# Optimization experiments

Measured on AMD Instinct MI355X. Metric: run time of the kernel, lower is better.

Reference implementation:

```python
import jax, jax.numpy as jnp
import numpy as np

N_NODES = 50000
N_EDGES = 1_600_000
F_IN = 128
HID = 64
HEADS = 4
NCLS = 2
NEG_SLOPE = 0.2  # PyG GATConv default


def setup_inputs() -> dict:
    key = jax.random.key(0)
    ks = jax.random.split(key, 12)
    s = 0.1
    return {
        "x": jax.random.normal(ks[0], (N_NODES, F_IN), jnp.float32),
        "edge_index": jax.random.randint(ks[1], (2, N_EDGES), 0, N_NODES, jnp.int32),
        "W1": jax.random.normal(ks[2], (F_IN, HEADS * HID), jnp.float32) * s,
        "att_src1": jax.random.normal(ks[3], (HEADS, HID), jnp.float32) * s,
        "att_dst1": jax.random.normal(ks[4], (HEADS, HID), jnp.float32) * s,
        "b1": jnp.zeros((HEADS * HID,), jnp.float32),
        "W2": jax.random.normal(ks[5], (HEADS * HID, HID), jnp.float32) * s,
        "att_src2": jax.random.normal(ks[6], (1, HID), jnp.float32) * s,
        "att_dst2": jax.random.normal(ks[7], (1, HID), jnp.float32) * s,
        "b2": jnp.zeros((HID,), jnp.float32),
        "Wc": jax.random.normal(ks[8], (HID, NCLS), jnp.float32) * s,
        "bc": jnp.zeros((NCLS,), jnp.float32),
    }


def _gat_layer(x, src, dst, W, a_src, a_dst, bias, heads, out_ch, concat):
    """Faithful PyG GATConv (eval mode): gather, LeakyReLU score, segment softmax by dst, scatter-add."""
    n = x.shape[0]
    h = (x @ W).reshape(n, heads, out_ch)            # [N, H, C]
    alpha_s = (h * a_src).sum(-1)                    # [N, H]
    alpha_d = (h * a_dst).sum(-1)                    # [N, H]
    e = jax.nn.leaky_relu(alpha_s[src] + alpha_d[dst], NEG_SLOPE)  # [E, H]
    e_max = jax.ops.segment_max(e, dst, num_segments=n)
    ex = jnp.exp(e - e_max[dst])
    denom = jax.ops.segment_sum(ex, dst, num_segments=n)
    coef = ex / (denom[dst] + 1e-16)                 # [E, H]
    out = jax.ops.segment_sum(h[src] * coef[:, :, None], dst, num_segments=n)  # [N, H, C]
    out = out.reshape(n, heads * out_ch) if concat else out.mean(axis=1)
    return out + bias


def reference(x, edge_index, W1, att_src1, att_dst1, b1, W2, att_src2, att_dst2, b2, Wc, bc):
    n = x.shape[0]
    loop = jnp.arange(n, dtype=edge_index.dtype)     # GATConv add_self_loops=True
    src = jnp.concatenate([edge_index[0], loop])
    dst = jnp.concatenate([edge_index[1], loop])
    h1 = jax.nn.elu(_gat_layer(x, src, dst, W1, att_src1, att_dst1, b1, HEADS, HID, True))
    # dropout p=0.6 is identity in eval mode
    h2 = jax.nn.elu(_gat_layer(h1, src, dst, W2, att_src2, att_dst2, b2, 1, HID, False))
    pooled = h2.mean(axis=0, keepdims=True)          # batch=None path: [1, HID]
    return pooled @ Wc + bc                          # [1, NCLS]
```

## Files before the change

### kernel.cpp

```cpp
#include <hip/hip_runtime.h>
#include <cstdint>
#include <cstddef>

#define NEG_SLOPE 0.2f
#define F_IN 128
#define C1 256
#define HID 64
#define HEADS 4
#define LOG2E 1.4426950408889634f
#define NBUCK 196
#define BCAP 10240

typedef __attribute__((ext_vector_type(8))) short bf16x8;
typedef __attribute__((ext_vector_type(4))) float f32x4;
typedef __attribute__((ext_vector_type(2))) float f32x2;

__device__ __forceinline__ float wave_reduce_sum(float v) {
#pragma unroll
  for (int off = 32; off > 0; off >>= 1) v += __shfl_down(v, off);
  return v;
}

__device__ __forceinline__ unsigned short f2bf(float f) {
  union { float f; unsigned int u; } v; v.f = f;
  unsigned int u = v.u;
  unsigned int r = (u + 0x7fffu + ((u >> 16) & 1u)) >> 16;
  return (unsigned short)r;
}
__device__ __forceinline__ float bf_lo(unsigned int u) { return __uint_as_float(u << 16); }
__device__ __forceinline__ float bf_hi(unsigned int u) { return __uint_as_float(u & 0xffff0000u); }

__device__ __forceinline__ unsigned char f2fp8(float f) {
  int p = __builtin_amdgcn_cvt_pk_fp8_f32(f, f, 0, false);
  return (unsigned char)(p & 0xff);
}

__global__ __launch_bounds__(256) void setup_kernel(const float* __restrict__ W1,
                                                    const float* __restrict__ W2,
                                                    unsigned short* __restrict__ W1b,
                                                    unsigned short* __restrict__ W2b,
                                                    int* __restrict__ gcursor,
                                                    float* __restrict__ poolrep) {
  const int TOT = 256 + 4096 + 32768 + 16384;
  for (int idx = threadIdx.x + blockIdx.x * 256; idx < TOT; idx += 256 * gridDim.x) {
    if (idx < 256) {
      gcursor[idx] = 0;
    } else if (idx < 256 + 4096) {
      poolrep[idx - 256] = 0.f;
    } else if (idx < 256 + 4096 + 32768) {
      int o = idx - (256 + 4096);
      int head = o >> 13, ks = (o >> 11) & 3, nt = (o >> 9) & 3;
      int lane = (o >> 3) & 63, j = o & 7;
      int k = ks * 32 + (lane >> 4) * 8 + j;
      int c = head * 64 + nt * 16 + (lane & 15);
      W1b[o] = f2bf(W1[k * 256 + c]);
    } else {
      int o = idx - (256 + 4096 + 32768);
      int ks = o >> 11, nt = (o >> 9) & 3, lane = (o >> 3) & 63, j = o & 7;
      int k = ks * 32 + (lane >> 4) * 8 + j;
      int c = nt * 16 + (lane & 15);
      W2b[o] = f2bf(W2[k * 64 + c]);
    }
  }
}

__global__ __launch_bounds__(256) void gemm1_mfma(const float* __restrict__ Af,
                                                  const unsigned short* __restrict__ Wb,
                                                  unsigned char* __restrict__ H8,
                                                  float* __restrict__ as_out,
                                                  float* __restrict__ ad_out,
                                                  const float* __restrict__ att_s,
                                                  const float* __restrict__ att_d,
                                                  int M) {
  constexpr int KSTEPS = 4, NH = HEADS, K = 128, N = 256;
  const int lane = threadIdx.x & 63, wid = threadIdx.x >> 6;
  const int rowbase = blockIdx.x * 64 + wid * 16;
  const int g = lane >> 4, li = lane & 15;
  int r_a = rowbase + li;
  if (r_a > M - 1) r_a = M - 1;

  f32x4 acc[NH][4];
#pragma unroll
  for (int h = 0; h < NH; h++)
#pragma unroll
    for (int nt = 0; nt < 4; nt++) {
      acc[h][nt][0] = 0.f; acc[h][nt][1] = 0.f; acc[h][nt][2] = 0.f; acc[h][nt][3] = 0.f;
    }

#pragma unroll
  for (int ks = 0; ks < KSTEPS; ks++) {
    bf16x8 a;
    const float* p = Af + (size_t)r_a * K + ks * 32 + g * 8;
    float4 v0 = *(const float4*)p, v1 = *(const float4*)(p + 4);
    a[0] = (short)f2bf(v0.x); a[1] = (short)f2bf(v0.y);
    a[2] = (short)f2bf(v0.z); a[3] = (short)f2bf(v0.w);
    a[4] = (short)f2bf(v1.x); a[5] = (short)f2bf(v1.y);
    a[6] = (short)f2bf(v1.z); a[7] = (short)f2bf(v1.w);
#pragma unroll
    for (int h = 0; h < NH; h++)
#pragma unroll
      for (int nt = 0; nt < 4; nt++) {
        bf16x8 b = *(const bf16x8*)(Wb + ((size_t)((h * KSTEPS + ks) * 4 + nt) * 64 + lane) * 8);
        acc[h][nt] = __builtin_amdgcn_mfma_f32_16x16x32_bf16(a, b, acc[h][nt], 0, 0, 0);
      }
  }

#pragma unroll
  for (int h = 0; h < NH; h++) {
    float asum[4] = {0.f, 0.f, 0.f, 0.f}, dsum[4] = {0.f, 0.f, 0.f, 0.f};
#pragma unroll
    for (int nt = 0; nt < 4; nt++) {
      float ws = att_s[h * 64 + nt * 16 + li];
      float wd = att_d[h * 64 + nt * 16 + li];
#pragma unroll
      for (int r = 0; r < 4; r++) { asum[r] += acc[h][nt][r] * ws; dsum[r] += acc[h][nt][r] * wd; }
    }
#pragma unroll
    for (int r = 0; r < 4; r++) {
#pragma unroll
      for (int m = 1; m < 16; m <<= 1) {
        asum[r] += __shfl_xor(asum[r], m);
        dsum[r] += __shfl_xor(dsum[r], m);
      }
    }
#pragma unroll
    for (int r = 0; r < 4; r++) {
      int gr = rowbase + g * 4 + r;
      if (gr < M) {
#pragma unroll
        for (int nt = 0; nt < 4; nt++)
          H8[(size_t)gr * N + h * 64 + nt * 16 + li] = f2fp8(acc[h][nt][r]);
        if (li == 0) {
          as_out[(size_t)gr * NH + h] = asum[r] * LOG2E;
          ad_out[(size_t)gr * NH + h] = dsum[r] * LOG2E;
        }
      }
    }
  }
}

__global__ __launch_bounds__(256) void partition_kernel(const int* __restrict__ esrc,
                                                        const int* __restrict__ edst,
                                                        int* __restrict__ gcursor,
                                                        int2* __restrict__ pairs,
                                                        int E, int Etot) {
  __shared__ int hist[256];
  __shared__ int base[256];
  const int tid = threadIdx.x;
  const int e0 = blockIdx.x * 2048;
  hist[tid] = 0;
  __syncthreads();
  int d8[8], rk8[8], bk8[8];
#pragma unroll
  for (int j = 0; j < 8; j++) {
    int e = e0 + tid * 8 + j;
    d8[j] = -1;
    if (e < Etot) {
      int d = (e < E) ? edst[e] : (e - E);
      d8[j] = d;
      bk8[j] = d >> 8;
      rk8[j] = atomicAdd(&hist[bk8[j]], 1);
    }
  }
  __syncthreads();
  if (hist[tid] > 0) base[tid] = atomicAdd(&gcursor[tid], hist[tid]);
  __syncthreads();
#pragma unroll
  for (int j = 0; j < 8; j++) {
    int e = e0 + tid * 8 + j;
    if (e < Etot) {
      int s = (e < E) ? esrc[e] : (e - E);
      int2 pr; pr.x = s; pr.y = d8[j];
      pairs[(size_t)bk8[j] * BCAP + base[bk8[j]] + rk8[j]] = pr;
    }
  }
}

__global__ __launch_bounds__(512) void bucket_csr(const int2* __restrict__ pairs,
                                                  const int* __restrict__ gcursor,
                                                  const float4* __restrict__ as1,
                                                  const float4* __restrict__ ad1,
                                                  int4* __restrict__ recs,
                                                  int* __restrict__ row_ptr,
                                                  int N, int Etot) {
  __shared__ int hist[256], offs[256], cnt2[256], gpre[256];
  const int b = blockIdx.x;
  const int tid = threadIdx.x;
  if (tid < 256) {
    hist[tid] = 0; cnt2[tid] = 0;
    gpre[tid] = (tid < NBUCK) ? gcursor[tid] : 0;
  }
  __syncthreads();
  for (int off = 1; off < 256; off <<= 1) {
    int t = 0;
    if (tid < 256 && tid >= off) t = gpre[tid - off];
    __syncthreads();
    if (tid < 256) gpre[tid] += t;
    __syncthreads();
  }
  const int cnt = gcursor[b];
  const int gbase = (b == 0) ? 0 : gpre[b - 1];
  const int2* bp = pairs + (size_t)b * BCAP;
  if (b == 0 && tid == 0) row_ptr[N] = Etot;

  for (int i = tid; i < cnt; i += 512) atomicAdd(&hist[bp[i].y & 255], 1);
  __syncthreads();
  if (tid < 256) offs[tid] = hist[tid];
  __syncthreads();
  for (int off = 1; off < 256; off <<= 1) {
    int t = 0;
    if (tid < 256 && tid >= off) t = offs[tid - off];
    __syncthreads();
    if (tid < 256) offs[tid] += t;
    __syncthreads();
  }
  if (tid < 256) {
    int node = b * 256 + tid;
    if (node < N) row_ptr[node] = gbase + offs[tid] - hist[tid];
  }
  __syncthreads();
  for (int i = tid; i < cnt; i += 512) {
    int2 pr = bp[i];
    int lo = pr.y & 255;
    int rank = atomicAdd(&cnt2[lo], 1);
    int pos = gbase + offs[lo] - hist[lo] + rank;
    float4 a = as1[pr.x], dd = ad1[pr.y];
    float s0 = a.x + dd.x, s1 = a.y + dd.y, s2 = a.z + dd.z, s3 = a.w + dd.w;
    float w0 = exp2f(fmaxf(s0, NEG_SLOPE * s0));
    float w1 = exp2f(fmaxf(s1, NEG_SLOPE * s1));
    float w2 = exp2f(fmaxf(s2, NEG_SLOPE * s2));
    float w3 = exp2f(fmaxf(s3, NEG_SLOPE * s3));
    int4 r;
    r.x = pr.x;
    r.y = (int)((unsigned)f2bf(w0) | ((unsigned)f2bf(w1) << 16));
    r.z = (int)((unsigned)f2bf(w2) | ((unsigned)f2bf(w3) << 16));
    r.w = 0;
    recs[pos] = r;
  }
}

__global__ __launch_bounds__(256) void agg1_gemm2(const unsigned char* __restrict__ H8,
                                                  const int4* __restrict__ recs,
                                                  const int* __restrict__ row_ptr,
                                                  const float* __restrict__ b1,
                                                  const unsigned short* __restrict__ W2b,
                                                  const float* __restrict__ att_s2,
                                                  const float* __restrict__ att_d2,
                                                  unsigned char* __restrict__ H2,
                                                  float* __restrict__ as2,
                                                  float* __restrict__ ad2, int n) {
  __shared__ unsigned char lds_h[16 * 512];
  __shared__ float pA[4][16], pD[4][16];
  const int tid = threadIdx.x;
  const int l = tid & 63, w = tid >> 6;
  const int dbase = blockIdx.x * 16;
  const int hh = l >> 4;
  const int shamt = (hh & 1) ? 0 : 16;
  const bool lowpair = hh < 2;
  const float4 bb = *(const float4*)(b1 + l * 4);

#define WSEL(r) __uint_as_float(((unsigned)((lowpair) ? (r).y : (r).z) << shamt) & 0xffff0000u)
#define ACCUM(wgt, u8)                                                     \
  {                                                                        \
    f32x2 lo_ = __builtin_amdgcn_cvt_pk_f32_fp8((int)(u8), false);         \
    f32x2 hi_ = __builtin_amdgcn_cvt_pk_f32_fp8((int)(u8), true);          \
    accA += lo_ * (wgt); accB += hi_ * (wgt);                              \
    denom += (wgt);                                                        \
  }
  for (int i = 0; i < 4; i++) {
    int dloc = w * 4 + i;
    int d = dbase + dloc;
    bool active = d < n;
    f32x2 accA = {0.f, 0.f}, accB = {0.f, 0.f};
    float denom = 0.f;
    if (active) {
      int e0 = __builtin_amdgcn_readfirstlane(row_ptr[d]);
      int e1 = __builtin_amdgcn_readfirstlane(row_ptr[d + 1]);
      int e = e0;
      for (; e + 3 < e1; e += 4) {
        int4 r0 = recs[e], r1 = recs[e + 1], r2 = recs[e + 2], r3 = recs[e + 3];
        unsigned u0 = *(const unsigned*)(H8 + (size_t)r0.x * C1 + l * 4);
        unsigned u1 = *(const unsigned*)(H8 + (size_t)r1.x * C1 + l * 4);
        unsigned u2 = *(const unsigned*)(H8 + (size_t)r2.x * C1 + l * 4);
        unsigned u3 = *(const unsigned*)(H8 + (size_t)r3.x * C1 + l * 4);
        float w0 = WSEL(r0), w1 = WSEL(r1), w2 = WSEL(r2), w3 = WSEL(r3);
        ACCUM(w0, u0) ACCUM(w1, u1) ACCUM(w2, u2) ACCUM(w3, u3)
      }
      for (; e < e1; e++) {
        int4 r0 = recs[e];
        unsigned u = *(const unsigned*)(H8 + (size_t)r0.x * C1 + l * 4);
        float wq = WSEL(r0);
        ACCUM(wq, u)
      }
    }
    float inv = 1.f / (denom + 1e-16f);
    float4 o;
    o.x = accA[0] * inv + bb.x; o.y = accA[1] * inv + bb.y;
    o.z = accB[0] * inv + bb.z; o.w = accB[1] * inv + bb.w;
    o.x = o.x > 0.f ? o.x : (__expf(o.x) - 1.f);
    o.y = o.y > 0.f ? o.y : (__expf(o.y) - 1.f);
    o.z = o.z > 0.f ? o.z : (__expf(o.z) - 1.f);
    o.w = o.w > 0.f ? o.w : (__expf(o.w) - 1.f);
    if (!active) { o.x = 0.f; o.y = 0.f; o.z = 0.f; o.w = 0.f; }
    uint2 pk;
    pk.x = (unsigned int)f2bf(o.x) | ((unsigned int)f2bf(o.y) << 16);
    pk.y = (unsigned int)f2bf(o.z) | ((unsigned int)f2bf(o.w) << 16);
    unsigned byte = (unsigned)(l * 8) ^ ((unsigned)(dloc & 7) << 4);
    *(uint2*)(lds_h + dloc * 512 + byte) = pk;
  }
#undef ACCUM
#undef WSEL
  __syncthreads();

  const int li2 = l & 15, g2 = l >> 4;
  f32x4 acc2;
  acc2[0] = 0.f; acc2[1] = 0.f; acc2[2] = 0.f; acc2[3] = 0.f;
#pragma unroll
  for (int ks = 0; ks < 8; ks++) {
    unsigned byte = (unsigned)((ks * 32 + g2 * 8) * 2) ^ ((unsigned)(li2 & 7) << 4);
    bf16x8 a = *(const bf16x8*)(lds_h + li2 * 512 + byte);
    bf16x8 b = *(const bf16x8*)(W2b + ((size_t)(ks * 4 + w) * 64 + l) * 8);
    acc2 = __builtin_amdgcn_mfma_f32_16x16x32_bf16(a, b, acc2, 0, 0, 0);
  }

  float ws = att_s2[w * 16 + li2], wd = att_d2[w * 16 + li2];
  float asum[4], dsum[4];
#pragma unroll
  for (int r = 0; r < 4; r++) { asum[r] = acc2[r] * ws; dsum[r] = acc2[r] * wd; }
#pragma unroll
  for (int r = 0; r < 4; r++) {
#pragma unroll
    for (int m = 1; m < 16; m <<= 1) {
      asum[r] += __shfl_xor(asum[r], m);
      dsum[r] += __shfl_xor(dsum[r], m);
    }
  }
#pragma unroll
  for (int r = 0; r < 4; r++) {
    int row = g2 * 4 + r;
    int d2 = dbase + row;
    if (d2 < n) H2[(size_t)d2 * HID + w * 16 + li2] = f2fp8(acc2[r]);
    if (li2 == 0) { pA[w][row] = asum[r]; pD[w][row] = dsum[r]; }
  }
  __syncthreads();
  if (tid < 16) {
    int d2 = dbase + tid;
    if (d2 < n) as2[d2] = (pA[0][tid] + pA[1][tid] + pA[2][tid] + pA[3][tid]) * LOG2E;
  } else if (tid < 32) {
    int row = tid - 16;
    int d2 = dbase + row;
    if (d2 < n) ad2[d2] = (pD[0][row] + pD[1][row] + pD[2][row] + pD[3][row]) * LOG2E;
  }
}

__global__ __launch_bounds__(256) void agg2_pool(const unsigned char* __restrict__ H2,
                                                 const float* __restrict__ as_,
                                                 const float* __restrict__ ad_,
                                                 const int* __restrict__ row_ptr,
                                                 const int4* __restrict__ recs,
                                                 const float* __restrict__ b2,
                                                 float* __restrict__ poolrep, int n) {
  __shared__ float lds[4][64];
  int wid = threadIdx.x >> 6;
  int d = blockIdx.x * 4 + wid;
  int l = threadIdx.x & 63, q = l >> 4, li = l & 15;
  float ad = ad_[d];
  int e0 = row_ptr[d], e1 = row_ptr[d + 1];
  f32x2 accA = {0.f, 0.f}, accB = {0.f, 0.f};
  float denom = 0.f;
  for (int e = e0 + q; e < e1; e += 4) {
    int s = ((const int*)recs)[(size_t)e * 4];
    float sc = as_[s] + ad;
    float w = exp2f(fmaxf(sc, NEG_SLOPE * sc));
    denom += w;
    unsigned u = *(const unsigned*)(H2 + (size_t)s * HID + li * 4);
    f32x2 lo_ = __builtin_amdgcn_cvt_pk_f32_fp8((int)u, false);
    f32x2 hi_ = __builtin_amdgcn_cvt_pk_f32_fp8((int)u, true);
    accA += lo_ * w; accB += hi_ * w;
  }
#pragma unroll
  for (int m = 16; m <= 32; m <<= 1) {
    accA[0] += __shfl_xor(accA[0], m); accA[1] += __shfl_xor(accA[1], m);
    accB[0] += __shfl_xor(accB[0], m); accB[1] += __shfl_xor(accB[1], m);
    denom += __shfl_xor(denom, m);
  }
  if (q == 0) {
    float inv = 1.f / (denom + 1e-16f);
    float o[4] = {accA[0] * inv + b2[li * 4], accA[1] * inv + b2[li * 4 + 1],
                  accB[0] * inv + b2[li * 4 + 2], accB[1] * inv + b2[li * 4 + 3]};
#pragma unroll
    for (int j = 0; j < 4; j++) {
      float v = o[j];
      lds[wid][li * 4 + j] = v > 0.f ? v : (__expf(v) - 1.f);
    }
  }
  __syncthreads();
  if (threadIdx.x < 64) {
    int c = threadIdx.x;
    float v = lds[0][c] + lds[1][c] + lds[2][c] + lds[3][c];
    atomicAdd(&poolrep[(blockIdx.x & 63) * 64 + c], v);
  }
}

__global__ __launch_bounds__(64) void head_kernel(const float* __restrict__ poolrep,
                                                  const float* __restrict__ Wc,
                                                  const float* __restrict__ bc,
                                                  float* __restrict__ out, float inv_n) {
  int l = threadIdx.x;
  float p = 0.f;
  for (int k = 0; k < 64; k++) p += poolrep[k * 64 + l];
  p *= inv_n;
  float o0 = wave_reduce_sum(p * Wc[l * 2 + 0]);
  float o1 = wave_reduce_sum(p * Wc[l * 2 + 1]);
  if (l == 0) { out[0] = o0 + bc[0]; out[1] = o1 + bc[1]; }
}

static inline size_t align256(size_t x) { return (x + 255) & ~(size_t)255; }

extern "C" void kernel_launch(void* const* d_in, const int* in_sizes, int n_in,
                              void* d_out, int out_size, void* d_ws, size_t ws_size,
                              hipStream_t stream) {
  const float* x        = (const float*)d_in[0];
  const int*   ei       = (const int*)d_in[1];
  const float* W1       = (const float*)d_in[2];
  const float* att_src1 = (const float*)d_in[3];
  const float* att_dst1 = (const float*)d_in[4];
  const float* b1       = (const float*)d_in[5];
  const float* W2       = (const float*)d_in[6];
  const float* att_src2 = (const float*)d_in[7];
  const float* att_dst2 = (const float*)d_in[8];
  const float* b2       = (const float*)d_in[9];
  const float* Wc       = (const float*)d_in[10];
  const float* bc       = (const float*)d_in[11];
  float* out = (float*)d_out;

  const int N = in_sizes[0] / F_IN;
  const int E = in_sizes[1] / 2;
  const int Etot = E + N;
  const int* ei_src = ei;
  const int* ei_dst = ei + E;

  char* w = (char*)d_ws;
  size_t off = 0;
  unsigned char* h1b8 = (unsigned char*)(w + off); off += align256((size_t)N * C1);
  unsigned char* h2b8 = (unsigned char*)(w + off); off += align256((size_t)N * HID);
  float* as1   = (float*)(w + off); off += align256((size_t)N * HEADS * 4);
  float* ad1   = (float*)(w + off); off += align256((size_t)N * HEADS * 4);
  float* as2   = (float*)(w + off); off += align256((size_t)N * 4);
  float* ad2   = (float*)(w + off); off += align256((size_t)N * 4);
  int* row_ptr = (int*)(w + off);   off += align256((size_t)(N + 1) * 4);
  int* gcursor = (int*)(w + off);   off += align256(256 * 4);
  float* poolrep = (float*)(w + off); off += align256(64 * 64 * 4);
  unsigned short* W1b = (unsigned short*)(w + off); off += align256(32768 * 2);
  unsigned short* W2b = (unsigned short*)(w + off); off += align256(16384 * 2);
  int2* pairs  = (int2*)(w + off);  off += align256((size_t)NBUCK * BCAP * 8);
  int4* recs   = (int4*)(w + off);  off += align256((size_t)Etot * 16);

  int nb4 = (N + 3) / 4;
  int rowblocks = (N + 63) / 64;
  int pblocks = (Etot + 2047) / 2048;
  int fblocks = (N + 15) / 16;

  setup_kernel<<<104, 256, 0, stream>>>(W1, W2, W1b, W2b, gcursor, poolrep);
  partition_kernel<<<pblocks, 256, 0, stream>>>(ei_src, ei_dst, gcursor, pairs, E, Etot);
  gemm1_mfma<<<rowblocks, 256, 0, stream>>>(x, W1b, h1b8, as1, ad1,
                                            att_src1, att_dst1, N);
  bucket_csr<<<NBUCK, 512, 0, stream>>>(pairs, gcursor,
                                        (const float4*)as1, (const float4*)ad1,
                                        recs, row_ptr, N, Etot);
  agg1_gemm2<<<fblocks, 256, 0, stream>>>(h1b8, recs, row_ptr, b1, W2b,
                                          att_src2, att_dst2, h2b8, as2, ad2, N);
  agg2_pool<<<nb4, 256, 0, stream>>>(h2b8, as2, ad2, row_ptr, recs, b2, poolrep, N);
  head_kernel<<<1, 64, 0, stream>>>(poolrep, Wc, bc, out, 1.0f / (float)N);
}
```

Baseline: 213.7 us.

## Compress edge records into 16-bit source and packed weight arrays

```diff
diff --git a/kernel.cpp b/kernel.cpp
--- a/kernel.cpp
+++ b/kernel.cpp
@@ -14,6 +14,7 @@
 typedef __attribute__((ext_vector_type(8))) short bf16x8;
 typedef __attribute__((ext_vector_type(4))) float f32x4;
 typedef __attribute__((ext_vector_type(2))) float f32x2;
+typedef unsigned long long ull;
 
 __device__ __forceinline__ float wave_reduce_sum(float v) {
 #pragma unroll
@@ -27,8 +28,6 @@
   unsigned int r = (u + 0x7fffu + ((u >> 16) & 1u)) >> 16;
   return (unsigned short)r;
 }
-__device__ __forceinline__ float bf_lo(unsigned int u) { return __uint_as_float(u << 16); }
-__device__ __forceinline__ float bf_hi(unsigned int u) { return __uint_as_float(u & 0xffff0000u); }
 
 __device__ __forceinline__ unsigned char f2fp8(float f) {
   int p = __builtin_amdgcn_cvt_pk_fp8_f32(f, f, 0, false);
@@ -142,7 +141,7 @@
 __global__ __launch_bounds__(256) void partition_kernel(const int* __restrict__ esrc,
                                                         const int* __restrict__ edst,
                                                         int* __restrict__ gcursor,
-                                                        int2* __restrict__ pairs,
+                                                        unsigned* __restrict__ pairs,
                                                         int E, int Etot) {
   __shared__ int hist[256];
   __shared__ int base[256];
@@ -170,17 +169,18 @@
     int e = e0 + tid * 8 + j;
     if (e < Etot) {
       int s = (e < E) ? esrc[e] : (e - E);
-      int2 pr; pr.x = s; pr.y = d8[j];
-      pairs[(size_t)bk8[j] * BCAP + base[bk8[j]] + rk8[j]] = pr;
-    }
-  }
-}
-
-__global__ __launch_bounds__(512) void bucket_csr(const int2* __restrict__ pairs,
+      unsigned pk = (unsigned)s | ((unsigned)(d8[j] & 255) << 16);
+      __builtin_nontemporal_store(pk, &pairs[(size_t)bk8[j] * BCAP + base[bk8[j]] + rk8[j]]);
+    }
+  }
+}
+
+__global__ __launch_bounds__(512) void bucket_csr(const unsigned* __restrict__ pairs,
                                                   const int* __restrict__ gcursor,
                                                   const float4* __restrict__ as1,
                                                   const float4* __restrict__ ad1,
-                                                  int4* __restrict__ recs,
+                                                  unsigned short* __restrict__ src16,
+                                                  ull* __restrict__ w4,
                                                   int* __restrict__ row_ptr,
                                                   int N, int Etot) {
   __shared__ int hist[256], offs[256], cnt2[256], gpre[256];
@@ -200,10 +200,13 @@
   }
   const int cnt = gcursor[b];
   const int gbase = (b == 0) ? 0 : gpre[b - 1];
-  const int2* bp = pairs + (size_t)b * BCAP;
+  const unsigned* bp = pairs + (size_t)b * BCAP;
   if (b == 0 && tid == 0) row_ptr[N] = Etot;
 
-  for (int i = tid; i < cnt; i += 512) atomicAdd(&hist[bp[i].y & 255], 1);
+  for (int i = tid; i < cnt; i += 512) {
+    unsigned p = __builtin_nontemporal_load(&bp[i]);
+    atomicAdd(&hist[p >> 16], 1);
+  }
   __syncthreads();
   if (tid < 256) offs[tid] = hist[tid];
   __syncthreads();
@@ -220,27 +223,27 @@
   }
   __syncthreads();
   for (int i = tid; i < cnt; i += 512) {
-    int2 pr = bp[i];
-    int lo = pr.y & 255;
+    unsigned p = __builtin_nontemporal_load(&bp[i]);
+    int lo = (int)(p >> 16);
+    int src = (int)(p & 0xffffu);
     int rank = atomicAdd(&cnt2[lo], 1);
     int pos = gbase + offs[lo] - hist[lo] + rank;
-    float4 a = as1[pr.x], dd = ad1[pr.y];
+    float4 a = as1[src], dd = ad1[b * 256 + lo];
     float s0 = a.x + dd.x, s1 = a.y + dd.y, s2 = a.z + dd.z, s3 = a.w + dd.w;
     float w0 = exp2f(fmaxf(s0, NEG_SLOPE * s0));
     float w1 = exp2f(fmaxf(s1, NEG_SLOPE * s1));
     float w2 = exp2f(fmaxf(s2, NEG_SLOPE * s2));
     float w3 = exp2f(fmaxf(s3, NEG_SLOPE * s3));
-    int4 r;
-    r.x = pr.x;
-    r.y = (int)((unsigned)f2bf(w0) | ((unsigned)f2bf(w1) << 16));
-    r.z = (int)((unsigned)f2bf(w2) | ((unsigned)f2bf(w3) << 16));
-    r.w = 0;
-    recs[pos] = r;
+    unsigned w01 = (unsigned)f2bf(w0) | ((unsigned)f2bf(w1) << 16);
+    unsigned w23 = (unsigned)f2bf(w2) | ((unsigned)f2bf(w3) << 16);
+    __builtin_nontemporal_store((unsigned short)src, &src16[pos]);
+    __builtin_nontemporal_store((ull)w01 | ((ull)w23 << 32), &w4[pos]);
   }
 }
 
 __global__ __launch_bounds__(256) void agg1_gemm2(const unsigned char* __restrict__ H8,
-                                                  const int4* __restrict__ recs,
+                                                  const unsigned short* __restrict__ src16,
+                                                  const ull* __restrict__ w4,
                                                   const int* __restrict__ row_ptr,
                                                   const float* __restrict__ b1,
                                                   const unsigned short* __restrict__ W2b,
@@ -259,7 +262,7 @@
   const bool lowpair = hh < 2;
   const float4 bb = *(const float4*)(b1 + l * 4);
 
-#define WSEL(r) __uint_as_float(((unsigned)((lowpair) ? (r).y : (r).z) << shamt) & 0xffff0000u)
+#define WSEL(wv) __uint_as_float((((lowpair) ? (unsigned)(wv) : (unsigned)((wv) >> 32)) << shamt) & 0xffff0000u)
 #define ACCUM(wgt, u8)                                                     \
   {                                                                        \
     f32x2 lo_ = __builtin_amdgcn_cvt_pk_f32_fp8((int)(u8), false);         \
@@ -278,18 +281,26 @@
       int e1 = __builtin_amdgcn_readfirstlane(row_ptr[d + 1]);
       int e = e0;
       for (; e + 3 < e1; e += 4) {
-        int4 r0 = recs[e], r1 = recs[e + 1], r2 = recs[e + 2], r3 = recs[e + 3];
-        unsigned u0 = *(const unsigned*)(H8 + (size_t)r0.x * C1 + l * 4);
-        unsigned u1 = *(const unsigned*)(H8 + (size_t)r1.x * C1 + l * 4);
-        unsigned u2 = *(const unsigned*)(H8 + (size_t)r2.x * C1 + l * 4);
-        unsigned u3 = *(const unsigned*)(H8 + (size_t)r3.x * C1 + l * 4);
-        float w0 = WSEL(r0), w1 = WSEL(r1), w2 = WSEL(r2), w3 = WSEL(r3);
+        unsigned s0 = __builtin_nontemporal_load(&src16[e]);
+        unsigned s1 = __builtin_nontemporal_load(&src16[e + 1]);
+        unsigned s2 = __builtin_nontemporal_load(&src16[e + 2]);
+        unsigned s3 = __builtin_nontemporal_load(&src16[e + 3]);
+        ull wv0 = __builtin_nontemporal_load(&w4[e]);
+        ull wv1 = __builtin_nontemporal_load(&w4[e + 1]);
+        ull wv2 = __builtin_nontemporal_load(&w4[e + 2]);
+        ull wv3 = __builtin_nontemporal_load(&w4[e + 3]);
+        unsigned u0 = *(const unsigned*)(H8 + (size_t)s0 * C1 + l * 4);
+        unsigned u1 = *(const unsigned*)(H8 + (size_t)s1 * C1 + l * 4);
+        unsigned u2 = *(const unsigned*)(H8 + (size_t)s2 * C1 + l * 4);
+        unsigned u3 = *(const unsigned*)(H8 + (size_t)s3 * C1 + l * 4);
+        float w0 = WSEL(wv0), w1 = WSEL(wv1), w2 = WSEL(wv2), w3 = WSEL(wv3);
         ACCUM(w0, u0) ACCUM(w1, u1) ACCUM(w2, u2) ACCUM(w3, u3)
       }
       for (; e < e1; e++) {
-        int4 r0 = recs[e];
-        unsigned u = *(const unsigned*)(H8 + (size_t)r0.x * C1 + l * 4);
-        float wq = WSEL(r0);
+        unsigned s0 = __builtin_nontemporal_load(&src16[e]);
+        ull wv = __builtin_nontemporal_load(&w4[e]);
+        unsigned u = *(const unsigned*)(H8 + (size_t)s0 * C1 + l * 4);
+        float wq = WSEL(wv);
         ACCUM(wq, u)
       }
     }
@@ -357,7 +368,7 @@
                                                  const float* __restrict__ as_,
                                                  const float* __restrict__ ad_,
                                                  const int* __restrict__ row_ptr,
-                                                 const int4* __restrict__ recs,
+                                                 const unsigned short* __restrict__ src16,
                                                  const float* __restrict__ b2,
                                                  float* __restrict__ poolrep, int n) {
   __shared__ float lds[4][64];
@@ -369,7 +380,7 @@
   f32x2 accA = {0.f, 0.f}, accB = {0.f, 0.f};
   float denom = 0.f;
   for (int e = e0 + q; e < e1; e += 4) {
-    int s = ((const int*)recs)[(size_t)e * 4];
+    int s = (int)__builtin_nontemporal_load(&src16[e]);
     float sc = as_[s] + ad;
     float w = exp2f(fmaxf(sc, NEG_SLOPE * sc));
     denom += w;
@@ -453,8 +464,9 @@
   float* poolrep = (float*)(w + off); off += align256(64 * 64 * 4);
   unsigned short* W1b = (unsigned short*)(w + off); off += align256(32768 * 2);
   unsigned short* W2b = (unsigned short*)(w + off); off += align256(16384 * 2);
-  int2* pairs  = (int2*)(w + off);  off += align256((size_t)NBUCK * BCAP * 8);
-  int4* recs   = (int4*)(w + off);  off += align256((size_t)Etot * 16);
+  unsigned* pairs = (unsigned*)(w + off); off += align256((size_t)NBUCK * BCAP * 4);
+  unsigned short* src16 = (unsigned short*)(w + off); off += align256((size_t)Etot * 2);
+  ull* w4      = (ull*)(w + off);   off += align256((size_t)Etot * 8);
 
   int nb4 = (N + 3) / 4;
   int rowblocks = (N + 63) / 64;
@@ -467,9 +479,9 @@
                                             att_src1, att_dst1, N);
   bucket_csr<<<NBUCK, 512, 0, stream>>>(pairs, gcursor,
                                         (const float4*)as1, (const float4*)ad1,
-                                        recs, row_ptr, N, Etot);
-  agg1_gemm2<<<fblocks, 256, 0, stream>>>(h1b8, recs, row_ptr, b1, W2b,
+                                        src16, w4, row_ptr, N, Etot);
+  agg1_gemm2<<<fblocks, 256, 0, stream>>>(h1b8, src16, w4, row_ptr, b1, W2b,
                                           att_src2, att_dst2, h2b8, as2, ad2, N);
-  agg2_pool<<<nb4, 256, 0, stream>>>(h2b8, as2, ad2, row_ptr, recs, b2, poolrep, N);
+  agg2_pool<<<nb4, 256, 0, stream>>>(h2b8, as2, ad2, row_ptr, src16, b2, poolrep, N);
   head_kernel<<<1, 64, 0, stream>>>(poolrep, Wc, bc, out, 1.0f / (float)N);
 }
```

New measurement: 326.1 us. +52.6%, slower.
